# Kernel tuning notes

Measured on AMD Instinct MI355X. Metric: run time of the kernel, lower is better.

## Reference

```python
import jax, jax.numpy as jnp
import numpy as np

D_MODEL = 1024
N_HEADS = 16
D_K = D_MODEL // N_HEADS
SCALE = float(np.sqrt(D_K))


def setup_inputs() -> dict:
    key = jax.random.key(0)
    ks = jax.random.split(key, 9)
    B, L, D = 2, 2048, D_MODEL
    # xavier_uniform with gain 1/sqrt(2): limit = gain*sqrt(6/(fan_in+fan_out))
    limit = (1.0 / np.sqrt(2.0)) * np.sqrt(6.0 / (D + D))
    def xav(k):
        return jax.random.uniform(k, (D, D), jnp.float32, -limit, limit)
    return {
        "query": jax.random.normal(ks[0], (B, L, D), jnp.float32),
        "key": jax.random.normal(ks[1], (B, L, D), jnp.float32),
        "value": jax.random.normal(ks[2], (B, L, D), jnp.float32),
        "mask": jax.random.randint(ks[3], (B, L), 0, 2, jnp.int32),
        "w_q": xav(ks[4]),
        "w_k": xav(ks[5]),
        "w_v": xav(ks[6]),
        "w_o": xav(ks[7]),
        "b_o": jnp.zeros((D,), jnp.float32),
    }


def reference(query, key, value, mask, w_q, w_k, w_v, w_o, b_o):
    B, L, D = query.shape
    H, dk = N_HEADS, D_K
    # torch Linear: x @ W.T ; reshape to (B, H, L, dk)
    def proj(x, w):
        return (x @ w.T).reshape(B, L, H, dk).transpose(0, 2, 1, 3)
    Q = proj(query, w_q)
    K = proj(key, w_k)
    V = proj(value, w_v)
    scores = jnp.einsum("bhqd,bhkd->bhqk", Q, K) / SCALE
    scores = scores.astype(jnp.float32)
    keep = (mask != 0)[:, None, None, :]  # (B,1,1,L)
    scores = jnp.where(keep, scores, jnp.float32(-10000.0))
    attn = jax.nn.softmax(scores, axis=-1).astype(Q.dtype)
    # dropout is identity in eval mode
    ctx = jnp.einsum("bhqk,bhkd->bhqd", attn, V)
    ctx = ctx.transpose(0, 2, 1, 3).reshape(B, L, D)
    return ctx @ w_o.T + b_o
```

## Files before the change

### kernel.cpp

```cpp
#include <hip/hip_runtime.h>

#define DMODEL 1024
#define NHEADS 16
#define BATCH  2
#define SEQ    2048
#define MROWS  (BATCH * SEQ)

typedef unsigned short u16;
typedef unsigned int   u32;
typedef __attribute__((ext_vector_type(8))) short short8v;
typedef __attribute__((ext_vector_type(4))) short short4v;
typedef __attribute__((ext_vector_type(4))) int   int4v;
typedef __attribute__((ext_vector_type(4))) float f32x4;

#define SCALE_LOG2E 0.18033688011112042f

__device__ inline float bf2f(u16 u) {
  union { u32 i; float f; } c; c.i = ((u32)u) << 16; return c.f;
}
__device__ inline u16 f2bf(float f) {
  union { float f; u32 i; } c; c.f = f;
  u32 r = c.i + 0x7fffu + ((c.i >> 16) & 1u);
  return (u16)(r >> 16);
}
__device__ inline short8v ld8(const u16* p) { return *(const short8v*)p; }
__device__ inline short8v cvt8f(const float* p) {
  f32x4 v0 = *(const f32x4*)p;
  f32x4 v1 = *(const f32x4*)(p + 4);
  short8v r;
#pragma unroll
  for (int j = 0; j < 4; ++j) { r[j] = (short)f2bf(v0[j]); r[4 + j] = (short)f2bf(v1[j]); }
  return r;
}
__device__ inline void gload_lds16(const u16* g, u16* l) {
  __builtin_amdgcn_global_load_lds(
      (const __attribute__((address_space(1))) void*)g,
      (__attribute__((address_space(3))) void*)l, 16, 0, 0);
}
__device__ inline float exp2raw(float x) { return __builtin_amdgcn_exp2f(x); }
__device__ inline u32 pkbf(float a, float b) {
  u32 d; asm("v_cvt_pk_bf16_f32 %0, %1, %2" : "=v"(d) : "v"(a), "v"(b));
  return d;
}

__device__ inline int swz(int idx) {
  return idx ^ ((((idx >> 6) ^ (idx >> 9)) & 7) << 3);
}

__global__ __launch_bounds__(256) void cvt_all(
    const float* __restrict__ xq, const float* __restrict__ xk,
    const float* __restrict__ xv, const float* __restrict__ wq,
    const float* __restrict__ wk, const float* __restrict__ wv,
    const float* __restrict__ wo, u16* __restrict__ dst)
{
  int b = blockIdx.x;
  const float* s;
  u16* d;
  int local;
  if (b < 6144) {
    int which = b >> 11;
    s = (which == 0) ? xq : (which == 1) ? xk : xv;
    d = dst + (long)which * 4194304;
    local = b & 2047;
  } else {
    int wb = b - 6144;
    int which = wb >> 9;
    s = (which == 0) ? wq : (which == 1) ? wk : (which == 2) ? wv : wo;
    d = dst + 12582912 + (long)which * 1048576;
    local = wb & 511;
  }
  const long idx = ((long)local * 256 + threadIdx.x) * 8;
  *(short8v*)(d + idx) = cvt8f(s + idx);
}

__global__ __launch_bounds__(256) void gemm_bf(
    const u16* __restrict__ A, const u16* __restrict__ W,
    void* __restrict__ Craw, const float* __restrict__ bias, int CF32,
    int Ndim, int Kdim)
{
  __shared__ __align__(16) u16 As[2][128 * 32];
  __shared__ __align__(16) u16 Bs[2][64 * 32];

  const int tid  = threadIdx.x;
  const int lane = tid & 63;
  const int w    = tid >> 6;
  const int wr   = w >> 1, wc = w & 1;
  const int r    = lane & 15, g = lane >> 4;

  const long brow = (long)blockIdx.x * 128;
  const long bcol = (long)blockIdx.y * 64;

  const int trow = tid >> 2;
  const int tk   = (tid & 3) * 8;

  const u16* Arow0 = A + (brow + trow) * (long)Kdim + tk;
  const u16* Arow1 = A + (brow + trow + 64) * (long)Kdim + tk;
  const u16* Wrow  = W + (bcol + trow) * (long)Kdim + tk;
  const int  woff  = w * 512;

  f32x4 acc[4][2] = {};

  gload_lds16(Arow0, As[0] + woff);
  gload_lds16(Arow1, As[0] + woff + 2048);
  gload_lds16(Wrow,  Bs[0] + woff);
  __syncthreads();

  int cur = 0;
  for (int k0 = 0; k0 < Kdim; k0 += 32) {
    if (k0 + 32 < Kdim) {
      gload_lds16(Arow0 + k0 + 32, As[cur ^ 1] + woff);
      gload_lds16(Arow1 + k0 + 32, As[cur ^ 1] + woff + 2048);
      gload_lds16(Wrow  + k0 + 32, Bs[cur ^ 1] + woff);
    }

    short8v afr[4], bfr[2];
#pragma unroll
    for (int m = 0; m < 4; ++m)
      afr[m] = ld8(As[cur] + (wr * 64 + m * 16 + r) * 32 + g * 8);
#pragma unroll
    for (int n = 0; n < 2; ++n)
      bfr[n] = ld8(Bs[cur] + (wc * 32 + n * 16 + r) * 32 + g * 8);
#pragma unroll
    for (int m = 0; m < 4; ++m)
#pragma unroll
      for (int n = 0; n < 2; ++n)
        acc[m][n] = __builtin_amdgcn_mfma_f32_16x16x32_bf16(afr[m], bfr[n], acc[m][n], 0, 0, 0);

    __syncthreads();
    cur ^= 1;
  }

#pragma unroll
  for (int n = 0; n < 2; ++n) {
    const long col = bcol + wc * 32 + n * 16 + r;
    const float bv = bias ? bias[col] : 0.0f;
#pragma unroll
    for (int m = 0; m < 4; ++m) {
#pragma unroll
      for (int r4 = 0; r4 < 4; ++r4) {
        const long row = brow + wr * 64 + m * 16 + g * 4 + r4;
        if (CF32) ((float*)Craw)[row * (long)Ndim + col] = acc[m][n][r4] + bv;
        else      ((u16*)Craw)[row * (long)Ndim + col]   = f2bf(acc[m][n][r4] + bv);
      }
    }
  }
}

__global__ __launch_bounds__(512) void attn_kernel(
    const u16* __restrict__ Q, const u16* __restrict__ K,
    const u16* __restrict__ V, const int* __restrict__ mask,
    u16* __restrict__ O)
{
  __shared__ __align__(16) u16 Ks[2][64 * 64];
  __shared__ __align__(16) u16 Vt[2][64 * 64];
  __shared__ __align__(16) u16 Ps[256 * 64];

  const int tid  = threadIdx.x;
  const int lane = tid & 63;
  const int w    = tid >> 6;
  const int r    = lane & 15, g = lane >> 4;

  const int slot = blockIdx.x;
  const int p    = (slot & 7) + 8 * (slot >> 6);
  const int x    = (slot >> 3) & 7;
  const int h    = p & 15;
  const int b    = p >> 4;

  const long wq = (long)b * SEQ + (long)x * 256 + w * 32;

  short8v qf[2][2];
#pragma unroll
  for (int qt = 0; qt < 2; ++qt)
#pragma unroll
    for (int ks = 0; ks < 2; ++ks)
      qf[qt][ks] = ld8(Q + (wq + qt * 16 + r) * DMODEL + h * 64 + ks * 32 + g * 8);

  f32x4 of[2][4] = {};
  float lsum[2] = {0.f, 0.f};

  const int trow = tid >> 3;
  const int td   = (tid & 7) * 8;

  const u16* Kb = K + (long)b * SEQ * DMODEL + h * 64;
  const u16* Vb = V + (long)b * SEQ * DMODEL + h * 64;
  const int* mb = mask + (long)b * SEQ;

  {
    short8v k0v = ld8(Kb + (long)trow * DMODEL + td);
    short8v v0v = ld8(Vb + (long)trow * DMODEL + td);
    *(short8v*)(Ks[0] + swz(trow * 64 + td)) = k0v;
#pragma unroll
    for (int j = 0; j < 8; ++j)
      Vt[0][swz((td + j) * 64 + trow)] = (u16)v0v[j];
  }

  int cur = 0;

  for (int t = 0; t < SEQ / 64; ++t) {
    const int kt0 = t * 64;
    const bool more = (t < SEQ / 64 - 1);

    int4v keepc[4];
#pragma unroll
    for (int kt = 0; kt < 4; ++kt)
      keepc[kt] = *(const int4v*)(mb + kt0 + kt * 16 + g * 4);

    short8v nk0, nv0;
    if (more) {
      nk0 = ld8(Kb + (long)(kt0 + 64 + trow) * DMODEL + td);
      nv0 = ld8(Vb + (long)(kt0 + 64 + trow) * DMODEL + td);
    }

    __syncthreads();

    const u16* Kc = Ks[cur];
    const u16* Vc = Vt[cur];

    f32x4 sf[2][4] = {};
#pragma unroll
    for (int ks = 0; ks < 2; ++ks) {
      short8v kf[4];
#pragma unroll
      for (int kt = 0; kt < 4; ++kt)
        kf[kt] = ld8(Kc + swz((kt * 16 + r) * 64 + ks * 32 + g * 8));
#pragma unroll
      for (int qt = 0; qt < 2; ++qt)
#pragma unroll
        for (int kt = 0; kt < 4; ++kt)
          sf[qt][kt] = __builtin_amdgcn_mfma_f32_16x16x32_bf16(kf[kt], qf[qt][ks], sf[qt][kt], 0, 0, 0);
    }

#pragma unroll
    for (int qt = 0; qt < 2; ++qt) {
      const int prow = (w * 32 + qt * 16 + r) * 64;
#pragma unroll
      for (int kt = 0; kt < 4; ++kt) {
        float p0 = keepc[kt][0] ? exp2raw(sf[qt][kt][0] * SCALE_LOG2E) : 0.f;
        float p1 = keepc[kt][1] ? exp2raw(sf[qt][kt][1] * SCALE_LOG2E) : 0.f;
        float p2 = keepc[kt][2] ? exp2raw(sf[qt][kt][2] * SCALE_LOG2E) : 0.f;
        float p3 = keepc[kt][3] ? exp2raw(sf[qt][kt][3] * SCALE_LOG2E) : 0.f;
        union { u32 u[2]; short4v s; } pk;
        pk.u[0] = pkbf(p0, p1);
        pk.u[1] = pkbf(p2, p3);
        *(short4v*)(Ps + swz(prow + kt * 16 + g * 4)) = pk.s;
        lsum[qt] += (p0 + p1) + (p2 + p3);
      }
    }

#pragma unroll
    for (int ks = 0; ks < 2; ++ks) {
      short8v vb[4];
#pragma unroll
      for (int dt = 0; dt < 4; ++dt)
        vb[dt] = ld8(Vc + swz((dt * 16 + r) * 64 + ks * 32 + g * 8));
#pragma unroll
      for (int qt = 0; qt < 2; ++qt) {
        short8v pa = ld8(Ps + swz((w * 32 + qt * 16 + r) * 64 + ks * 32 + g * 8));
#pragma unroll
        for (int dt = 0; dt < 4; ++dt)
          of[qt][dt] = __builtin_amdgcn_mfma_f32_16x16x32_bf16(pa, vb[dt], of[qt][dt], 0, 0, 0);
      }
    }

    if (more) {
      *(short8v*)(Ks[cur ^ 1] + swz(trow * 64 + td)) = nk0;
#pragma unroll
      for (int j = 0; j < 8; ++j)
        Vt[cur ^ 1][swz((td + j) * 64 + trow)] = (u16)nv0[j];
      cur ^= 1;
    }
  }

#pragma unroll
  for (int qt = 0; qt < 2; ++qt) {
    float s = lsum[qt];
    s += __shfl_xor(s, 16);
    s += __shfl_xor(s, 32);
#pragma unroll
    for (int r4 = 0; r4 < 4; ++r4) {
      const float d = __shfl(s, g * 4 + r4);
      const float rcp = (d > 0.f) ? (1.0f / d) : 0.0f;
#pragma unroll
      for (int dt = 0; dt < 4; ++dt) {
        const long row = wq + qt * 16 + g * 4 + r4;
        const int  col = h * 64 + dt * 16 + r;
        O[row * DMODEL + col] = f2bf(of[qt][dt][r4] * rcp);
      }
    }
  }
}

extern "C" void kernel_launch(void* const* d_in, const int* in_sizes, int n_in,
                              void* d_out, int out_size, void* d_ws, size_t ws_size,
                              hipStream_t stream) {
  const float* q_in = (const float*)d_in[0];
  const float* k_in = (const float*)d_in[1];
  const float* v_in = (const float*)d_in[2];
  const int*   mask = (const int*)d_in[3];
  const float* w_q  = (const float*)d_in[4];
  const float* w_k  = (const float*)d_in[5];
  const float* w_v  = (const float*)d_in[6];
  const float* w_o  = (const float*)d_in[7];
  const float* b_o  = (const float*)d_in[8];

  u16* S  = (u16*)d_ws;
  u16* Xq = S;
  u16* Xk = S + 4194304;
  u16* Xv = S + 8388608;
  u16* WQ = S + 12582912;
  u16* WK = S + 13631488;
  u16* WV = S + 14680064;
  u16* WO = S + 15728640;
  u16* Qw = (u16*)d_out;
  u16* Kw = Xq;
  u16* Vw = Xk;
  u16* Cw = Xv;

  dim3 blk(256);

  cvt_all<<<dim3(8192), blk, 0, stream>>>(q_in, k_in, v_in, w_q, w_k, w_v, w_o, S);

  dim3 ggrid(MROWS / 128, DMODEL / 64);
  gemm_bf<<<ggrid, blk, 0, stream>>>(Xq, WQ, Qw, nullptr, 0, DMODEL, DMODEL);
  gemm_bf<<<ggrid, blk, 0, stream>>>(Xk, WK, Kw, nullptr, 0, DMODEL, DMODEL);
  gemm_bf<<<ggrid, blk, 0, stream>>>(Xv, WV, Vw, nullptr, 0, DMODEL, DMODEL);

  attn_kernel<<<dim3(256), dim3(512), 0, stream>>>(Qw, Kw, Vw, mask, Cw);

  gemm_bf<<<ggrid, blk, 0, stream>>>(Cw, WO, (float*)d_out, b_o, 1, DMODEL, DMODEL);
}
```

Baseline: 151.2 us.

## Batch QKV projections into one launch and double GEMM k-tile depth

The three Q/K/V projection GEMMs are merged into a single launch using blockIdx.z to select the operand set, which removes two launches and fills the GPU with a larger grid. The GEMM k-step also grows from 32 to 64, with each stage split into two 32-wide halves, so there are half as many barriers and prefetch rounds. In exchange, LDS use per block doubles, which may reduce occupancy.

```diff
diff --git a/kernel.cpp b/kernel.cpp
--- a/kernel.cpp
+++ b/kernel.cpp
@@ -74,12 +74,18 @@
 }
 
 __global__ __launch_bounds__(256) void gemm_bf(
-    const u16* __restrict__ A, const u16* __restrict__ W,
-    void* __restrict__ Craw, const float* __restrict__ bias, int CF32,
-    int Ndim, int Kdim)
+    const u16* __restrict__ A0, const u16* __restrict__ A1, const u16* __restrict__ A2,
+    const u16* __restrict__ W0, const u16* __restrict__ W1, const u16* __restrict__ W2,
+    void* __restrict__ C0, void* __restrict__ C1, void* __restrict__ C2,
+    const float* __restrict__ bias, int CF32, int Ndim, int Kdim)
 {
-  __shared__ __align__(16) u16 As[2][128 * 32];
-  __shared__ __align__(16) u16 Bs[2][64 * 32];
+  __shared__ __align__(16) u16 As[2][128 * 64];
+  __shared__ __align__(16) u16 Bs[2][64 * 64];
+
+  const int z = blockIdx.z;
+  const u16* A = (z == 0) ? A0 : (z == 1) ? A1 : A2;
+  const u16* W = (z == 0) ? W0 : (z == 1) ? W1 : W2;
+  void* Craw   = (z == 0) ? C0 : (z == 1) ? C1 : C2;
 
   const int tid  = threadIdx.x;
   const int lane = tid & 63;
@@ -100,31 +106,43 @@
 
   f32x4 acc[4][2] = {};
 
-  gload_lds16(Arow0, As[0] + woff);
-  gload_lds16(Arow1, As[0] + woff + 2048);
-  gload_lds16(Wrow,  Bs[0] + woff);
+  gload_lds16(Arow0,      As[0] + woff);
+  gload_lds16(Arow1,      As[0] + woff + 2048);
+  gload_lds16(Arow0 + 32, As[0] + woff + 4096);
+  gload_lds16(Arow1 + 32, As[0] + woff + 6144);
+  gload_lds16(Wrow,       Bs[0] + woff);
+  gload_lds16(Wrow + 32,  Bs[0] + woff + 2048);
   __syncthreads();
 
   int cur = 0;
-  for (int k0 = 0; k0 < Kdim; k0 += 32) {
-    if (k0 + 32 < Kdim) {
-      gload_lds16(Arow0 + k0 + 32, As[cur ^ 1] + woff);
-      gload_lds16(Arow1 + k0 + 32, As[cur ^ 1] + woff + 2048);
-      gload_lds16(Wrow  + k0 + 32, Bs[cur ^ 1] + woff);
-    }
-
-    short8v afr[4], bfr[2];
-#pragma unroll
-    for (int m = 0; m < 4; ++m)
-      afr[m] = ld8(As[cur] + (wr * 64 + m * 16 + r) * 32 + g * 8);
-#pragma unroll
-    for (int n = 0; n < 2; ++n)
-      bfr[n] = ld8(Bs[cur] + (wc * 32 + n * 16 + r) * 32 + g * 8);
-#pragma unroll
-    for (int m = 0; m < 4; ++m)
+  for (int k0 = 0; k0 < Kdim; k0 += 64) {
+    if (k0 + 64 < Kdim) {
+      const int kn = k0 + 64;
+      gload_lds16(Arow0 + kn,      As[cur ^ 1] + woff);
+      gload_lds16(Arow1 + kn,      As[cur ^ 1] + woff + 2048);
+      gload_lds16(Arow0 + kn + 32, As[cur ^ 1] + woff + 4096);
+      gload_lds16(Arow1 + kn + 32, As[cur ^ 1] + woff + 6144);
+      gload_lds16(Wrow + kn,       Bs[cur ^ 1] + woff);
+      gload_lds16(Wrow + kn + 32,  Bs[cur ^ 1] + woff + 2048);
+    }
+
+#pragma unroll
+    for (int half = 0; half < 2; ++half) {
+      const u16* Ah = As[cur] + half * 4096;
+      const u16* Bh = Bs[cur] + half * 2048;
+      short8v afr[4], bfr[2];
+#pragma unroll
+      for (int m = 0; m < 4; ++m)
+        afr[m] = ld8(Ah + (wr * 64 + m * 16 + r) * 32 + g * 8);
 #pragma unroll
       for (int n = 0; n < 2; ++n)
-        acc[m][n] = __builtin_amdgcn_mfma_f32_16x16x32_bf16(afr[m], bfr[n], acc[m][n], 0, 0, 0);
+        bfr[n] = ld8(Bh + (wc * 32 + n * 16 + r) * 32 + g * 8);
+#pragma unroll
+      for (int m = 0; m < 4; ++m)
+#pragma unroll
+        for (int n = 0; n < 2; ++n)
+          acc[m][n] = __builtin_amdgcn_mfma_f32_16x16x32_bf16(afr[m], bfr[n], acc[m][n], 0, 0, 0);
+    }
 
     __syncthreads();
     cur ^= 1;
@@ -320,12 +338,14 @@
 
   cvt_all<<<dim3(8192), blk, 0, stream>>>(q_in, k_in, v_in, w_q, w_k, w_v, w_o, S);
 
-  dim3 ggrid(MROWS / 128, DMODEL / 64);
-  gemm_bf<<<ggrid, blk, 0, stream>>>(Xq, WQ, Qw, nullptr, 0, DMODEL, DMODEL);
-  gemm_bf<<<ggrid, blk, 0, stream>>>(Xk, WK, Kw, nullptr, 0, DMODEL, DMODEL);
-  gemm_bf<<<ggrid, blk, 0, stream>>>(Xv, WV, Vw, nullptr, 0, DMODEL, DMODEL);
+  dim3 pgrid(MROWS / 128, DMODEL / 64, 3);
+  gemm_bf<<<pgrid, blk, 0, stream>>>(Xq, Xk, Xv, WQ, WK, WV,
+                                     Qw, Kw, Vw, nullptr, 0, DMODEL, DMODEL);
 
   attn_kernel<<<dim3(256), dim3(512), 0, stream>>>(Qw, Kw, Vw, mask, Cw);
 
-  gemm_bf<<<ggrid, blk, 0, stream>>>(Cw, WO, (float*)d_out, b_o, 1, DMODEL, DMODEL);
-}
+  dim3 ggrid(MROWS / 128, DMODEL / 64, 1);
+  gemm_bf<<<ggrid, blk, 0, stream>>>(Cw, Cw, Cw, WO, WO, WO,
+                                     (float*)d_out, (float*)d_out, (float*)d_out,
+                                     b_o, 1, DMODEL, DMODEL);
+}
```

Measured after the change: 127.1 us. -15.9%, faster.
